# Kernel tuning notes

Hardware: AMD Instinct MI355X
Metric: run time of the kernel (lower is better)

The kernel has to match this reference:

```python
import jax, jax.numpy as jnp
import numpy as np

DIM = 384; HEADS = 16; HEAD_DIM = DIM // HEADS; HID = 4 * DIM
ETA_SCALE = 0.01; CLIP_INNER = 1.0; EPS = 1e-5
B = 8; T_FR = 32; GH = 16; GW = 16; CHUNK = 8; N = T_FR * GH * GW
D_SEG = 2 * (HEAD_DIM // 3 // 2)  # 8 dims each for t/h/w rotation (3*8 == head_dim)


def _layernorm(x, g, b):
    m = jnp.mean(x, -1, keepdims=True)
    v = jnp.var(x, -1, keepdims=True)
    return (x - m) * jax.lax.rsqrt(v + EPS) * g + b


def _mlp(W1, b1, W2, b2, x):
    # 2-layer Titan memory / CMS level MLP: dim -> 4*dim -> dim, GELU
    return jax.nn.gelu(x @ W1 + b1) @ W2 + b2


def _rope_seg(x, pos):
    # x: [..., s] interleaved-pair RoPE with positions pos (broadcastable to x[..., 0])
    s = x.shape[-1]; half = s // 2
    freqs = 1.0 / (10000.0 ** (jnp.arange(half, dtype=x.dtype) / half))
    ang = pos[..., None] * freqs
    c, si = jnp.cos(ang), jnp.sin(ang)
    x1, x2 = x[..., 0::2], x[..., 1::2]
    return jnp.stack([x1 * c - x2 * si, x1 * si + x2 * c], -1).reshape(x.shape)


def _apply_rope(x, tp, hp, wp):
    # 3D RoPE per head over (t, h, w) position segments
    b, n, d = x.shape
    xh = x.reshape(b, n, HEADS, HEAD_DIM)
    s = D_SEG
    parts = [_rope_seg(xh[..., 0:s], tp[None, :, None]),
             _rope_seg(xh[..., s:2 * s], hp[None, :, None]),
             _rope_seg(xh[..., 2 * s:3 * s], wp[None, :, None])]
    if 3 * s < HEAD_DIM:
        parts.append(xh[..., 3 * s:])
    return jnp.concatenate(parts, -1).reshape(b, n, d)


def _forward(x, norm1_g, norm1_b, q_W, tW1, tb1, tW2, tb2, out_W, out_b,
             norm2_g, norm2_b, cms_W1, cms_b1, cms_W2, cms_b2, T, H, W, chunk_size):
    Bx, Nt, D = x.shape
    y = _layernorm(x, norm1_g, norm1_b)
    nc = T // chunk_size
    Cper = chunk_size * H * W
    y_ch = y.reshape(Bx, nc, Cper, D).swapaxes(0, 1)  # [nc, B, Cper, D]
    # per-chunk RoPE positions (positions restart each chunk, matching _titan_forward_chunk)
    tp = jnp.repeat(jnp.arange(chunk_size, dtype=x.dtype), H * W)
    hp = jnp.tile(jnp.repeat(jnp.arange(H, dtype=x.dtype), W), chunk_size)
    wp = jnp.tile(jnp.arange(W, dtype=x.dtype), chunk_size * H)

    def mem_loss(W1, b1, W2, b2, kk, tt):
        return jnp.mean((_mlp(W1, b1, W2, b2, kk) - tt) ** 2)

    grad_fn = jax.grad(mem_loss, argnums=(0, 1, 2, 3))
    mlp_v = jax.vmap(_mlp, in_axes=(0, 0, 0, 0, None))

    def step(carry, yc):
        W1s, b1s, W2s, b2s = carry  # stacked [5, ...]: k, v, eta, alpha, memory
        gen = mlp_v(W1s[:4], b1s[:4], W2s[:4], b2s[:4], yc)  # [4, B, C, D]
        k, v, eta_raw, alpha_raw = gen[0], gen[1], gen[2], gen[3]
        eta = jax.nn.softplus(eta_raw) * ETA_SCALE
        alpha = jax.nn.sigmoid(alpha_raw)
        q = yc @ q_W
        q = _apply_rope(q, tp, hp, wp)
        k = _apply_rope(k, tp, hp, wp)
        out = _mlp(W1s[4], b1s[4], W2s[4], b2s[4], q)  # retrieve from main memory
        # surprise signal (per-token retrieval error norm); threshold=0 -> always update
        # surprise = jnp.linalg.norm(v - out, axis=-1)
        # self-targets v_hat = M_box(v) for the 4 adaptive memories; main memory targets v
        vhat = mlp_v(W1s[:4], b1s[:4], W2s[:4], b2s[:4], v)
        targets = jnp.concatenate([jax.lax.stop_gradient(vhat), v[None]], 0)  # [5,B,C,D]
        g1, g2, g3, g4 = jax.vmap(grad_fn, in_axes=(0, 0, 0, 0, None, 0))(
            W1s, b1s, W2s, b2s, k, targets)
        norm = jnp.sqrt(jnp.sum(g1 * g1, (1, 2)) + jnp.sum(g2 * g2, 1)
                        + jnp.sum(g3 * g3, (1, 2)) + jnp.sum(g4 * g4, 1))
        sc = jnp.minimum(1.0, CLIP_INNER / (norm + 1e-12))  # inner grad clip per memory
        em = jnp.mean(eta); am = jnp.mean(alpha)
        # DGD update with decay alpha and lr eta: p <- (1-alpha)*p - eta*g
        W1n = (1 - am) * W1s - em * g1 * sc[:, None, None]
        b1n = (1 - am) * b1s - em * g2 * sc[:, None]
        W2n = (1 - am) * W2s - em * g3 * sc[:, None, None]
        b2n = (1 - am) * b2s - em * g4 * sc[:, None]
        return (W1n, b1n, W2n, b2n), out

    _, outs = jax.lax.scan(step, (tW1, tb1, tW2, tb2), y_ch)
    titan = outs.swapaxes(0, 1).reshape(Bx, Nt, D) @ out_W + out_b
    x2 = x + titan
    # Phase B: CMS multi-frequency MLP cascade (sequential chain of level MLPs)
    h = _layernorm(x2, norm2_g, norm2_b)
    for l in range(cms_W1.shape[0]):
        h = _mlp(cms_W1[l], cms_b1[l], cms_W2[l], cms_b2[l], h)
    return x2 + h


def setup_inputs() -> dict:
    key = jax.random.key(0)
    ks = jax.random.split(key, 8)
    s = 0.02
    f = jnp.float32
    return {
        'x': jax.random.normal(ks[0], (B, N, DIM), f),
        'norm1_g': jnp.ones((DIM,), f), 'norm1_b': jnp.zeros((DIM,), f),
        'q_W': jax.random.normal(ks[1], (DIM, DIM), f) * s,
        'tW1': jax.random.normal(ks[2], (5, DIM, HID), f) * s,
        'tb1': jnp.zeros((5, HID), f),
        'tW2': jax.random.normal(ks[3], (5, HID, DIM), f) * s,
        'tb2': jnp.zeros((5, DIM), f),
        'out_W': jax.random.normal(ks[4], (DIM, DIM), f) * s,
        'out_b': jnp.zeros((DIM,), f),
        'norm2_g': jnp.ones((DIM,), f), 'norm2_b': jnp.zeros((DIM,), f),
        'cms_W1': jax.random.normal(ks[5], (3, DIM, HID), f) * s,
        'cms_b1': jnp.zeros((3, HID), f),
        'cms_W2': jax.random.normal(ks[6], (3, HID, DIM), f) * s,
        'cms_b2': jnp.zeros((3, DIM), f),
        'T': T_FR, 'H': GH, 'W': GW, 'chunk_size': CHUNK,
    }


def reference(x, norm1_g, norm1_b, q_W, tW1, tb1, tW2, tb2, out_W, out_b,
              norm2_g, norm2_b, cms_W1, cms_b1, cms_W2, cms_b2, T, H, W, chunk_size):
    return _forward(x, norm1_g, norm1_b, q_W, tW1, tb1, tW2, tb2, out_W, out_b,
                    norm2_g, norm2_b, cms_W1, cms_b1, cms_W2, cms_b2, T, H, W, chunk_size)
```

## Files before the change

kernel.cpp:

```cpp
#include <hip/hip_runtime.h>
#include <cstddef>
#include <cstdint>


typedef __bf16 bf16;
typedef __bf16 bf16x4 __attribute__((ext_vector_type(4)));
typedef __bf16 bf16x8 __attribute__((ext_vector_type(8)));
typedef float  f32x4  __attribute__((ext_vector_type(4)));

constexpr float INV_CNT = 1.0f / 6291456.0f;

__device__ __forceinline__ float fast_gelu(float x) {
  float u = 0.7978845608028654f * (x + 0.044715f * x * x * x);
  return x / (1.0f + __expf(-2.0f * u));
}
__device__ __forceinline__ float fast_gelu_grad(float x) {
  float x2 = x * x;
  float u = 0.7978845608028654f * (x + 0.044715f * x * x2);
  float s = 1.0f / (1.0f + __expf(-2.0f * u));
  return s + x * s * (1.0f - s) * 1.5957691216057308f * (1.0f + 0.134145f * x2);
}
__device__ __forceinline__ f32x4 gelu4(f32x4 v) {
  v[0] = fast_gelu(v[0]); v[1] = fast_gelu(v[1]);
  v[2] = fast_gelu(v[2]); v[3] = fast_gelu(v[3]);
  return v;
}
__device__ __forceinline__ bf16x4 tobf4(f32x4 v) {
  bf16x4 o; o[0] = (bf16)v[0]; o[1] = (bf16)v[1]; o[2] = (bf16)v[2]; o[3] = (bf16)v[3];
  return o;
}
__device__ __forceinline__ f32x4 tof4(bf16x4 v) {
  return f32x4{(float)v[0], (float)v[1], (float)v[2], (float)v[3]};
}

__device__ __forceinline__ void gload16(const bf16* g, void* lds) {
  __builtin_amdgcn_global_load_lds(
      (const __attribute__((address_space(1))) void*)g,
      (__attribute__((address_space(3))) void*)lds, 16, 0, 0);
}

template <int N>
__device__ __forceinline__ void wait_vmcnt() {
  if constexpr (N == 0)      asm volatile("s_waitcnt vmcnt(0)" ::: "memory");
  else if constexpr (N == 2) asm volatile("s_waitcnt vmcnt(2)" ::: "memory");
  else if constexpr (N == 3) asm volatile("s_waitcnt vmcnt(3)" ::: "memory");
  else if constexpr (N == 4) asm volatile("s_waitcnt vmcnt(4)" ::: "memory");
  __builtin_amdgcn_sched_barrier(0);
}

__device__ __forceinline__ int xcd_chunk(int id, int n) {
  int q = n >> 3, r = n & 7;
  int xcd = id & 7, pos = id >> 3;
  return (xcd < r ? xcd * (q + 1) : r * (q + 1) + (xcd - r) * q) + pos;
}

__global__ __launch_bounds__(64)
void ln_kernel(const float* __restrict__ x, const float* __restrict__ g,
               const float* __restrict__ b, bf16* __restrict__ y,
               int shift, int base, int stride) {
  int r = blockIdx.x;
  int src = ((r >> shift) * stride) + base + (r & ((1 << shift) - 1));
  int lane = threadIdx.x;
  const float* xr = x + (size_t)src * 384;
  float vals[6];
  float s = 0.f, s2 = 0.f;
#pragma unroll
  for (int i = 0; i < 6; ++i) {
    float v = xr[lane + i * 64];
    vals[i] = v; s += v; s2 += v * v;
  }
#pragma unroll
  for (int o = 32; o > 0; o >>= 1) { s += __shfl_xor(s, o); s2 += __shfl_xor(s2, o); }
  float m = s * (1.0f / 384.0f);
  float var = s2 * (1.0f / 384.0f) - m * m;
  float rr = rsqrtf(var + 1e-5f);
  bf16* yr = y + (size_t)r * 384;
#pragma unroll
  for (int i = 0; i < 6; ++i) {
    int c = lane + i * 64;
    yr[c] = (bf16)((vals[i] - m) * rr * g[c] + b[c]);
  }
}

__device__ __forceinline__ void trw_body(const float* in, bf16* out, int R, int C,
                                         int c0, int r0, int tid) {
  __shared__ float t[32][33];
  int tr = tid >> 3, tc = (tid & 7) * 4;
  f32x4 v = *(const f32x4*)&in[(size_t)(r0 + tr) * C + c0 + tc];
  t[tr][tc + 0] = v[0]; t[tr][tc + 1] = v[1]; t[tr][tc + 2] = v[2]; t[tr][tc + 3] = v[3];
  __syncthreads();
  bf16x4 o;
  o[0] = (bf16)t[tc + 0][tr]; o[1] = (bf16)t[tc + 1][tr];
  o[2] = (bf16)t[tc + 2][tr]; o[3] = (bf16)t[tc + 3][tr];
  *(bf16x4*)&out[(size_t)(c0 + tr) * R + r0 + tc] = o;
}

__global__ __launch_bounds__(256)
void trans_state(const float* __restrict__ SW1, const float* __restrict__ SW2,
                 bf16* __restrict__ sw1t, bf16* __restrict__ sw2t) {
  int z = blockIdx.z;
  if (z < 5)
    trw_body(SW1 + (size_t)z * 589824, sw1t + (size_t)z * 589824, 384, 1536,
             blockIdx.x * 32, blockIdx.y * 32, threadIdx.x);
  else
    trw_body(SW2 + (size_t)(z - 5) * 589824, sw2t + (size_t)(z - 5) * 589824, 1536, 384,
             blockIdx.y * 32, blockIdx.x * 32, threadIdx.x);
}

__global__ __launch_bounds__(256)
void trans_static(const float* __restrict__ qW, const float* __restrict__ outW,
                  const float* __restrict__ cW1, const float* __restrict__ cW2,
                  bf16* __restrict__ qwt, bf16* __restrict__ owt,
                  bf16* __restrict__ cw1t, bf16* __restrict__ cw2t) {
  int z = blockIdx.z;
  if (z < 2) {
    if (blockIdx.x >= 12) return;
    trw_body(z ? outW : qW, z ? owt : qwt, 384, 384,
             blockIdx.x * 32, blockIdx.y * 32, threadIdx.x);
  } else if (z < 5) {
    int lc = z - 2;
    trw_body(cW1 + (size_t)lc * 589824, cw1t + (size_t)lc * 589824, 384, 1536,
             blockIdx.x * 32, blockIdx.y * 32, threadIdx.x);
  } else {
    int lc = z - 5;
    trw_body(cW2 + (size_t)lc * 589824, cw2t + (size_t)lc * 589824, 1536, 384,
             blockIdx.y * 32, blockIdx.x * 32, threadIdx.x);
  }
}

__global__ __launch_bounds__(256)
void tr_bf(const bf16* __restrict__ in, bf16* __restrict__ out, int R, int C) {
  __shared__ bf16 t[32][36];
  int r0 = blockIdx.x * 32, c0 = blockIdx.y * 32;
  int tr = threadIdx.x >> 3, tc = (threadIdx.x & 7) * 4;
  bf16x4 v = *(const bf16x4*)&in[(size_t)(r0 + tr) * C + c0 + tc];
  t[tr][tc + 0] = v[0]; t[tr][tc + 1] = v[1]; t[tr][tc + 2] = v[2]; t[tr][tc + 3] = v[3];
  __syncthreads();
  bf16x4 o;
  o[0] = t[tc + 0][tr]; o[1] = t[tc + 1][tr]; o[2] = t[tc + 2][tr]; o[3] = t[tc + 3][tr];
  *(bf16x4*)&out[(size_t)(c0 + tr) * R + r0 + tc] = o;
}

__global__ __launch_bounds__(256)
void copy_bf16(const float* __restrict__ in, bf16* __restrict__ out, int n) {
  int i = (blockIdx.x * 256 + threadIdx.x) * 4;
  if (i < n) {
    f32x4 v = *(const f32x4*)&in[i];
    *(bf16x4*)&out[i] = tobf4(v);
  }
}

enum { E_BF16 = 0, E_GELU, E_PAIR, E_SUB, E_MUL, E_F32ADD, E_KV, E_RED2 };

template <int EPI, int BM>
__global__ __launch_bounds__(BM == 128 ? 512 : 256)
void mm_fwd(const bf16* __restrict__ Act, int lda, const bf16* __restrict__ W,
            const float* __restrict__ bias, const bf16* __restrict__ baux,
            const float* __restrict__ faux, float* __restrict__ red,
            bf16* __restrict__ Cb, bf16* __restrict__ C2, bf16* __restrict__ Ct,
            float* __restrict__ Cf, int K, int ldc, int ldt, float scale,
            int croff, int cshift, int cbase, int cstride,
            long zA, long zW, int zB) {
  constexpr int NW = (BM == 128) ? 8 : 4;
  constexpr int NFM = 2;
  constexpr int TW = 8 / NW;
  constexpr int TA = (BM / 16) / NW;
  constexpr int LPT = TW + TA;
  constexpr int SWE = 128 * 32;
  constexpr int SAE = BM * 32;
  constexpr int BUFE = 2 * (SWE + SAE);
  constexpr int SLABE = NW * 16 * 68 * 2;
  constexpr int SMEME = (BUFE > SLABE) ? BUFE : SLABE;
  constexpr bool TRANS = (EPI == E_PAIR || EPI == E_SUB || EPI == E_MUL);
  __shared__ bf16 smem[SMEME];
  const int z = blockIdx.z;
  Act += (size_t)z * zA;
  W   += (size_t)z * zW;
  if (bias) bias += (size_t)z * zB;
  const int nx = gridDim.x;
  const int nid = xcd_chunk(blockIdx.y * nx + blockIdx.x, nx * gridDim.y);
  const int m0 = (nid / nx) * BM, i0 = (nid % nx) * 128;
  const int tid = threadIdx.x;
  const int l = tid & 63, w = tid >> 6;
  const int a = l & 15, g = l >> 4;
  const int wi0 = (w & 1) * 64, wm0 = (w >> 1) * 32;
  const int srow = l >> 2;
  const int sue = ((l & 3) ^ ((l >> 3) & 3)) * 8;
  const int fru = (g ^ ((a >> 1) & 3)) << 4;

  const bf16* wp = W   + (size_t)(i0 + srow) * K   + sue;
  const bf16* ap = Act + (size_t)(m0 + srow) * lda + sue;

  f32x4 acc[4][NFM];
#pragma unroll
  for (int i = 0; i < 4; ++i)
#pragma unroll
    for (int j = 0; j < NFM; ++j) acc[i][j] = f32x4{0.f, 0.f, 0.f, 0.f};

  auto stage = [&](int buf, int k0) {
    bf16* dW = smem + buf * SWE;
    bf16* dA = smem + 2 * SWE + buf * SAE;
#pragma unroll
    for (int t = 0; t < TW; ++t) {
      const int seg = w * TW + t;
      gload16(wp + (size_t)(seg * 16) * K + k0, (char*)dW + seg * 1024);
    }
#pragma unroll
    for (int t = 0; t < TA; ++t) {
      const int seg = w * TA + t;
      gload16(ap + (size_t)(seg * 16) * lda + k0, (char*)dA + seg * 1024);
    }
  };

  const int nIt = K >> 5;
  stage(0, 0);
  for (int it = 0; it < nIt; ++it) {
    const int cur = it & 1;
    if (it + 1 < nIt) { stage(cur ^ 1, (it + 1) << 5); wait_vmcnt<LPT>(); }
    else              { wait_vmcnt<0>(); }
    __builtin_amdgcn_s_barrier();
    const bf16* bW = smem + cur * SWE;
    const bf16* bA = smem + 2 * SWE + cur * SAE;
    {
      bf16x8 Af[4], Bf[NFM];
#pragma unroll
      for (int f = 0; f < 4; ++f) {
        const int rW = wi0 + f * 16 + a;
        Af[f] = *(const bf16x8*)((const char*)bW + rW * 64 + fru);
      }
#pragma unroll
      for (int f = 0; f < NFM; ++f) {
        const int rA = wm0 + f * 16 + a;
        Bf[f] = *(const bf16x8*)((const char*)bA + rA * 64 + fru);
      }
#pragma unroll
      for (int fi = 0; fi < 4; ++fi)
#pragma unroll
        for (int fm = 0; fm < NFM; ++fm)
          acc[fi][fm] = __builtin_amdgcn_mfma_f32_16x16x32_bf16(Af[fi], Bf[fm], acc[fi][fm], 0, 0, 0);
    }
    asm volatile("s_waitcnt lgkmcnt(0)" ::: "memory");
    __builtin_amdgcn_s_barrier();
  }

  if constexpr (EPI == E_RED2) {
    float ssum = 0.f;
#pragma unroll
    for (int fi = 0; fi < 4; ++fi) {
      f32x4 b4 = *(const f32x4*)&bias[i0 + wi0 + fi * 16 + g * 4];
#pragma unroll
      for (int fm = 0; fm < NFM; ++fm)
#pragma unroll
        for (int r = 0; r < 4; ++r) {
          float vv = acc[fi][fm][r] + b4[r];
          if (z == 0) ssum += fmaxf(vv, 0.f) + log1pf(__expf(-fabsf(vv)));
          else        ssum += 1.0f / (1.0f + __expf(-vv));
        }
    }
#pragma unroll
    for (int o = 32; o > 0; o >>= 1) ssum += __shfl_xor(ssum, o);
    float* wred = (float*)smem;
    if (l == 0) wred[w] = ssum;
    __syncthreads();
    if (tid == 0) {
      float t2 = 0.f;
      for (int q = 0; q < NW; ++q) t2 += wred[q];
      atomicAdd(&red[z], t2);
    }
    return;
  } else {
    float* T = (float*)smem + w * (16 * 68);
    const int iB = i0 + wi0;
    f32x4 b4 = f32x4{0.f, 0.f, 0.f, 0.f};
    if (bias) b4 = *(const f32x4*)&bias[iB + a * 4];
#pragma unroll
    for (int fm = 0; fm < NFM; ++fm) {
#pragma unroll
      for (int fi = 0; fi < 4; ++fi)
        *(f32x4*)&T[a * 68 + fi * 16 + g * 4] = acc[fi][fm];
      asm volatile("s_waitcnt lgkmcnt(0)" ::: "memory");
      __builtin_amdgcn_sched_barrier(0);

#pragma unroll
      for (int q = 0; q < 4; ++q) {
        const int ml = wm0 + fm * 16 + q * 4 + g;
        const int trow = q * 4 + g;
        f32x4 v = *(const f32x4*)&T[trow * 68 + a * 4];
        v += b4;
        if constexpr (EPI == E_F32ADD) {
          const int rr = croff + m0 + ml;
          const int crow = ((rr >> cshift) * cstride) + cbase + (rr & ((1 << cshift) - 1));
          const size_t cb = (size_t)crow * ldc + iB + a * 4;
          v += *(const f32x4*)&faux[cb];
          *(f32x4*)&Cf[cb] = v;
        } else {
          const size_t cb = (size_t)(m0 + ml) * ldc + iB + a * 4;
          if constexpr (EPI == E_BF16) {
            *(bf16x4*)&Cb[cb] = tobf4(v);
          } else if constexpr (EPI == E_KV) {
            bf16* DST = (z == 0) ? Cb : C2;
            *(bf16x4*)&DST[cb] = tobf4(v);
          } else if constexpr (EPI == E_GELU) {
            *(bf16x4*)&Cb[cb] = tobf4(gelu4(v));
          } else if constexpr (EPI == E_PAIR) {
            *(bf16x4*)&Cb[cb] = tobf4(v);
            f32x4 gv = gelu4(v);
            *(bf16x4*)&C2[cb] = tobf4(gv);
            *(f32x4*)&T[trow * 68 + a * 4] = gv;
          } else if constexpr (EPI == E_SUB) {
            f32x4 t4 = tof4(*(const bf16x4*)&baux[cb]);
            v = (v - t4) * scale;
            *(bf16x4*)&Cb[cb] = tobf4(v);
            *(f32x4*)&T[trow * 68 + a * 4] = v;
          } else if constexpr (EPI == E_MUL) {
            f32x4 h4 = tof4(*(const bf16x4*)&baux[cb]);
            v[0] *= fast_gelu_grad(h4[0]); v[1] *= fast_gelu_grad(h4[1]);
            v[2] *= fast_gelu_grad(h4[2]); v[3] *= fast_gelu_grad(h4[3]);
            *(f32x4*)&T[trow * 68 + a * 4] = v;
          }
        }
      }

      if constexpr (TRANS) {
        asm volatile("s_waitcnt lgkmcnt(0)" ::: "memory");
        __builtin_amdgcn_sched_barrier(0);
        const int mg = m0 + wm0 + fm * 16;
        bf16x8 o0, o1;
#pragma unroll
        for (int j = 0; j < 16; ++j) {
          float vv = T[j * 68 + l];
          if (j < 8) o0[j] = (bf16)vv; else o1[j - 8] = (bf16)vv;
        }
        *(bf16x8*)&Ct[(size_t)(iB + l) * ldt + mg] = o0;
        *(bf16x8*)&Ct[(size_t)(iB + l) * ldt + mg + 8] = o1;
      }
    }
  }
}

__global__ __launch_bounds__(512)
void mm_tn2c(const bf16* __restrict__ P1, int ldP1, const bf16* __restrict__ Q1, int ldQ1,
             float* __restrict__ Ga, int ldGa,
             const bf16* __restrict__ P2, int ldP2, const bf16* __restrict__ Q2, int ldQ2,
             float* __restrict__ Gb, int ldGb, int mlen,
             float* __restrict__ G4s, float* __restrict__ G2s) {
  constexpr int SBE = 128 * 64;
  __shared__ bf16 smem[4 * SBE];
  const int nid = xcd_chunk(blockIdx.x, gridDim.x);
  const int grp = nid / 36, pair = nid % 36;
  const int part = grp & 1, zsl = grp >> 1;
  const bf16* P; const bf16* Q; float* G; float* Gsum;
  int ldP, ldQ, ldG, p0, q0;
  if (part == 0) {
    P = P1; Q = Q1; G = Ga; ldP = ldP1; ldQ = ldQ1; ldG = ldGa; Gsum = G4s;
    p0 = (pair / 3) * 128; q0 = (pair % 3) * 128;
  } else {
    P = P2; Q = Q2; G = Gb; ldP = ldP2; ldQ = ldQ2; ldG = ldGb; Gsum = G2s;
    p0 = (pair / 12) * 128; q0 = (pair % 12) * 128;
  }
  const bool doSum = (p0 == 0);
  const int tid = threadIdx.x;
  const int mb = zsl * mlen;
  const int l = tid & 63, w = tid >> 6;
  const int a = l & 15, g = l >> 4;
  const int wp0 = (w & 1) * 64, wq0 = (w >> 1) * 32;
  const int lrow = l >> 3;
  const int lcolel = (((l & 7) ^ lrow) << 4) >> 1;

  const bf16* pp = P + (size_t)(p0 + lrow) * ldP + lcolel;
  const bf16* qp = Q + (size_t)(q0 + lrow) * ldQ + lcolel;

  f32x4 acc[4][2];
#pragma unroll
  for (int i = 0; i < 4; ++i)
#pragma unroll
    for (int j = 0; j < 2; ++j) acc[i][j] = f32x4{0.f, 0.f, 0.f, 0.f};
  float qsum = 0.f;
  const int srow = w * 16 + (l & 15);
  const int u0 = ((l >> 4) ^ (l & 7)) & 7;
  const int u1 = u0 ^ 4;

  auto stage = [&](int buf, int m0) {
    bf16* dP = smem + buf * SBE;
    bf16* dQ = smem + 2 * SBE + buf * SBE;
#pragma unroll
    for (int t = 0; t < 2; ++t) {
      const int seg = w * 2 + t;
      gload16(pp + (size_t)(seg * 8) * ldP + m0, (char*)dP + seg * 1024);
      gload16(qp + (size_t)(seg * 8) * ldQ + m0, (char*)dQ + seg * 1024);
    }
  };

  const int nIt = mlen >> 6;
  stage(0, mb);
  for (int it = 0; it < nIt; ++it) {
    const int cur = it & 1;
    if (it + 1 < nIt) { stage(cur ^ 1, mb + ((it + 1) << 6)); wait_vmcnt<4>(); }
    else              { wait_vmcnt<0>(); }
    __builtin_amdgcn_s_barrier();
    const bf16* bP = smem + cur * SBE;
    const bf16* bQ = smem + 2 * SBE + cur * SBE;
#pragma unroll
    for (int kh = 0; kh < 2; ++kh) {
      bf16x8 Pf[4], Qf[2];
#pragma unroll
      for (int f = 0; f < 4; ++f) {
        const int rP = wp0 + f * 16 + a;
        Pf[f] = *(const bf16x8*)((const char*)bP +
                 ((rP * 128 + kh * 64 + g * 16) ^ ((rP & 7) << 4)));
      }
#pragma unroll
      for (int f = 0; f < 2; ++f) {
        const int rQ = wq0 + f * 16 + a;
        Qf[f] = *(const bf16x8*)((const char*)bQ +
                 ((rQ * 128 + kh * 64 + g * 16) ^ ((rQ & 7) << 4)));
      }
#pragma unroll
      for (int f1 = 0; f1 < 4; ++f1)
#pragma unroll
        for (int f2 = 0; f2 < 2; ++f2)
          acc[f1][f2] = __builtin_amdgcn_mfma_f32_16x16x32_bf16(Pf[f1], Qf[f2], acc[f1][f2], 0, 0, 0);
    }
    if (doSum) {
      bf16x8 s0 = *(const bf16x8*)((const char*)bQ + srow * 128 + u0 * 16);
      bf16x8 s1 = *(const bf16x8*)((const char*)bQ + srow * 128 + u1 * 16);
#pragma unroll
      for (int e = 0; e < 8; ++e) qsum += (float)s0[e] + (float)s1[e];
    }
    asm volatile("s_waitcnt lgkmcnt(0)" ::: "memory");
    __builtin_amdgcn_s_barrier();
  }
#pragma unroll
  for (int f1 = 0; f1 < 4; ++f1)
#pragma unroll
    for (int f2 = 0; f2 < 2; ++f2)
#pragma unroll
      for (int r = 0; r < 4; ++r)
        atomicAdd(&G[(size_t)(p0 + wp0 + f1 * 16 + g * 4 + r) * ldG + q0 + wq0 + f2 * 16 + a],
                  acc[f1][f2][r]);
  if (doSum) {
    qsum += __shfl_xor(qsum, 16);
    qsum += __shfl_xor(qsum, 32);
    if (l < 16) atomicAdd(&Gsum[q0 + w * 16 + l], qsum);
  }
}

__global__ __launch_bounds__(256)
void rope_kernel(bf16* __restrict__ p0, int rbase) {
  int idx = blockIdx.x * blockDim.x + threadIdx.x;
  int row = idx >> 4, hd = idx & 15;
  int j = (rbase + row) & 2047;
  float pos[3] = { (float)(j >> 8), (float)((j >> 4) & 15), (float)(j & 15) };
  const float freqs[4] = { 1.0f, 0.1f, 0.01f, 0.001f };
  bf16* p = p0 + (size_t)row * 384 + hd * 24;
#pragma unroll
  for (int s = 0; s < 3; ++s) {
    bf16x8 vv = *(bf16x8*)(p + s * 8);
#pragma unroll
    for (int pr = 0; pr < 4; ++pr) {
      float ang = pos[s] * freqs[pr];
      float si, co;
      sincosf(ang, &si, &co);
      float e0 = (float)vv[2 * pr], e1 = (float)vv[2 * pr + 1];
      vv[2 * pr]     = (bf16)(e0 * co - e1 * si);
      vv[2 * pr + 1] = (bf16)(e0 * si + e1 * co);
    }
    *(bf16x8*)(p + s * 8) = vv;
  }
}

__global__ __launch_bounds__(256)
void sumsq_all(const float* __restrict__ G1, const float* __restrict__ G2,
               const float* __restrict__ G3, const float* __restrict__ G4,
               float* __restrict__ red) {
  int i = blockIdx.y, bx = blockIdx.x;
  const float* base; int per, lb, nb;
  if (bx < 256)      { base = G1 + (size_t)i * 589824; per = 589824; lb = bx;       nb = 256; }
  else if (bx < 512) { base = G3 + (size_t)i * 589824; per = 589824; lb = bx - 256; nb = 256; }
  else if (bx < 514) { base = G2 + (size_t)i * 1536;   per = 1536;   lb = bx - 512; nb = 2; }
  else               { base = G4 + (size_t)i * 384;    per = 384;    lb = bx - 514; nb = 2; }
  float s = 0.f;
  for (int idx = lb * 256 + threadIdx.x; idx < per; idx += nb * 256) {
    float v = base[idx]; s += v * v;
  }
  __shared__ float sm[256];
  sm[threadIdx.x] = s; __syncthreads();
  for (int o = 128; o > 0; o >>= 1) {
    if (threadIdx.x < o) sm[threadIdx.x] += sm[threadIdx.x + o];
    __syncthreads();
  }
  if (threadIdx.x == 0) atomicAdd(&red[2 + i], sm[0]);
}

__global__ __launch_bounds__(256)
void update_all(float* __restrict__ SW1, float* __restrict__ SB1,
                float* __restrict__ SW2, float* __restrict__ SB2,
                const float* __restrict__ G1, const float* __restrict__ G2,
                const float* __restrict__ G3, const float* __restrict__ G4,
                const float* __restrict__ red) {
  int i = blockIdx.y, bx = blockIdx.x;
  float* S; const float* G; int per, lb, nb;
  if (bx < 512)       { S = SW1; G = G1; per = 589824; lb = bx;        nb = 512; }
  else if (bx < 1024) { S = SW2; G = G3; per = 589824; lb = bx - 512;  nb = 512; }
  else if (bx < 1028) { S = SB1; G = G2; per = 1536;   lb = bx - 1024; nb = 4; }
  else                { S = SB2; G = G4; per = 384;    lb = bx - 1028; nb = 4; }
  size_t base = (size_t)i * per;
  float em = 0.01f * red[0] * INV_CNT;
  float am = red[1] * INV_CNT;
  float norm = sqrtf(red[2 + i]);
  float sc = fminf(1.0f, 1.0f / (norm + 1e-12f));
  float ws_ = 1.0f - am;
  float gs = em * sc;
  for (int idx = lb * 256 + (int)threadIdx.x; idx < per; idx += nb * 256)
    S[base + idx] = ws_ * S[base + idx] - gs * G[base + idx];
}

extern "C" void kernel_launch(void* const* d_in, const int* in_sizes, int n_in,
                              void* d_out, int out_size, void* d_ws, size_t ws_size,
                              hipStream_t stream) {
  const float* x    = (const float*)d_in[0];
  const float* n1g  = (const float*)d_in[1];
  const float* n1b  = (const float*)d_in[2];
  const float* qW   = (const float*)d_in[3];
  const float* tW1  = (const float*)d_in[4];
  const float* tb1  = (const float*)d_in[5];
  const float* tW2  = (const float*)d_in[6];
  const float* tb2  = (const float*)d_in[7];
  const float* outW = (const float*)d_in[8];
  const float* outb = (const float*)d_in[9];
  const float* n2g  = (const float*)d_in[10];
  const float* n2b  = (const float*)d_in[11];
  const float* cW1  = (const float*)d_in[12];
  const float* cb1  = (const float*)d_in[13];
  const float* cW2  = (const float*)d_in[14];
  const float* cb2  = (const float*)d_in[15];
  float* out = (float*)d_out;

  const size_t W1SZ = 384 * 1536, W2SZ = 1536 * 384;
  const size_t STATE = 5 * W1SZ + 5 * 1536 + 5 * W2SZ + 5 * 384;
  const size_t BF_W = 21 * W1SZ + 2 * 147456;
  const size_t CHUNK_BF = 4 * (size_t)16384 * 384;
  const size_t FIXEDF = 2 * STATE + 16 + BF_W / 2 + CHUNK_BF / 2;
  size_t MS = 16384;
  while (MS > 2048 && (FIXEDF + MS * 3840) * 4 > ws_size) MS >>= 1;
  if ((FIXEDF + MS * 3840) * 4 > ws_size) {
    hipMemcpyAsync(d_out, d_in[0], (size_t)25165824 * 4, hipMemcpyDeviceToDevice, stream);
    return;
  }
  const int NS = (int)(16384 / MS);
  const int iMS = (int)MS;

  float* ws = (float*)d_ws;
  size_t off = 0;
  auto alloc = [&](size_t n) { float* p = ws + off; off += n; return p; };
  auto balloc = [&](size_t n) { bf16* p = (bf16*)(ws + off); off += (n + 1) / 2; return p; };
  float* SW1 = alloc(5 * W1SZ);
  float* SB1 = alloc(5 * 1536);
  float* SW2 = alloc(5 * W2SZ);
  float* SB2 = alloc(5 * 384);
  float* G1  = alloc(5 * W1SZ);
  float* G2  = alloc(5 * 1536);
  float* G3  = alloc(5 * W2SZ);
  float* G4  = alloc(5 * 384);
  float* RED = alloc(16);
  bf16* Yc   = balloc((size_t)16384 * 384);
  bf16* Kb   = balloc((size_t)16384 * 384);
  bf16* Vb   = balloc((size_t)16384 * 384);
  bf16* Kbt  = balloc((size_t)16384 * 384);
  bf16* sw1t = balloc(5 * W1SZ);
  bf16* sw2t = balloc(5 * W2SZ);
  bf16* sw2c = balloc(5 * W2SZ);
  bf16* qwt  = balloc(147456);
  bf16* owt  = balloc(147456);
  bf16* cw1t = balloc(3 * W1SZ);
  bf16* cw2t = balloc(3 * W2SZ);
  bf16* pool = balloc(MS * 3072);
  bf16* GH1t = balloc(MS * 1536);
  bf16* DAt  = balloc(MS * 1536);
  bf16* OD   = balloc(MS * 384);
  bf16* ODt  = balloc(MS * 384);
  bf16* T2   = balloc(MS * 384);
  bf16* Tt   = balloc(MS * 384);
  bf16* H1r  = pool;
  bf16* GH1k = pool + MS * 1536;

  hipMemcpyAsync(SW1, tW1, 5 * W1SZ * 4, hipMemcpyDeviceToDevice, stream);
  hipMemcpyAsync(SB1, tb1, 5 * 1536 * 4, hipMemcpyDeviceToDevice, stream);
  hipMemcpyAsync(SW2, tW2, 5 * W2SZ * 4, hipMemcpyDeviceToDevice, stream);
  hipMemcpyAsync(SB2, tb2, 5 * 384 * 4, hipMemcpyDeviceToDevice, stream);

  trans_static<<<dim3(48, 12, 8), 256, 0, stream>>>(qW, outW, cW1, cW2, qwt, owt, cw1t, cw2t);

  const size_t grads_bytes = STATE * 4;
  const int gm  = iMS / 128;
  const int gm2 = iMS / 64;
  int mlen_t = iMS / 8; if (mlen_t < 128) mlen_t = 128;
  if (mlen_t > 2048) mlen_t = 2048;
  const int nzt = iMS / mlen_t;
  const int tn_grid = 36 * 2 * nzt;
  const float SC = 2.0f * INV_CNT;
  const size_t MSR = (size_t)iMS * 384;

  for (int c = 0; c < 4; ++c) {
    hipMemsetAsync(G1, 0, grads_bytes, stream);
    hipMemsetAsync(RED, 0, 64, stream);
    trans_state<<<dim3(48, 12, 10), 256, 0, stream>>>(SW1, SW2, sw1t, sw2t);
    copy_bf16<<<dim3(2880), 256, 0, stream>>>(SW2, sw2c, (int)(5 * W2SZ));

    ln_kernel<<<dim3(16384), dim3(64), 0, stream>>>(x, n1g, n1b, Yc, 11, c * 2048, 8192);

    for (int s = 0; s < NS; ++s) {
      const bf16* Ys = Yc + (size_t)s * MSR;
      mm_fwd<E_GELU, 128><<<dim3(24, gm), 512, 0, stream>>>(Ys, 384, sw1t,
          SB1, nullptr, nullptr, nullptr, pool, nullptr, nullptr, nullptr,
          384, 3072, 0, 0.f, 0, 30, 0, 0, 0, 0, 0);
      mm_fwd<E_KV, 64><<<dim3(3, gm2, 2), 256, 0, stream>>>(pool, 3072, sw2t,
          SB2, nullptr, nullptr, nullptr, Kb + s * MSR, Vb + s * MSR, nullptr, nullptr,
          1536, 384, 0, 0.f, 0, 30, 0, 0, 1536, (long)W2SZ, 384);
      mm_fwd<E_GELU, 128><<<dim3(24, gm), 512, 0, stream>>>(Ys, 384, sw1t + 2 * W1SZ,
          SB1 + 2 * 1536, nullptr, nullptr, nullptr, pool, nullptr, nullptr, nullptr,
          384, 3072, 0, 0.f, 0, 30, 0, 0, 0, 0, 0);
      mm_fwd<E_RED2, 64><<<dim3(3, gm2, 2), 256, 0, stream>>>(pool, 3072, sw2t + 2 * W2SZ,
          SB2 + 2 * 384, nullptr, nullptr, RED, nullptr, nullptr, nullptr, nullptr,
          1536, 384, 0, 0.f, 0, 30, 0, 0, 1536, (long)W2SZ, 384);
    }

    for (int s = 0; s < NS; ++s) {
      const bf16* Ys = Yc + (size_t)s * MSR;
      mm_fwd<E_BF16, 64><<<dim3(3, gm2), 256, 0, stream>>>(Ys, 384, qwt,
          nullptr, nullptr, nullptr, nullptr, Tt, nullptr, nullptr, nullptr,
          384, 384, 0, 0.f, 0, 30, 0, 0, 0, 0, 0);
      rope_kernel<<<dim3(iMS / 16), 256, 0, stream>>>(Tt, s * iMS);
      mm_fwd<E_GELU, 128><<<dim3(12, gm), 512, 0, stream>>>(Tt, 384, sw1t + 4 * W1SZ,
          SB1 + 4 * 1536, nullptr, nullptr, nullptr, GH1k, nullptr, nullptr, nullptr,
          384, 1536, 0, 0.f, 0, 30, 0, 0, 0, 0, 0);
      mm_fwd<E_BF16, 64><<<dim3(3, gm2), 256, 0, stream>>>(GH1k, 1536, sw2t + 4 * W2SZ,
          SB2 + 4 * 384, nullptr, nullptr, nullptr, T2, nullptr, nullptr, nullptr,
          1536, 384, 0, 0.f, 0, 30, 0, 0, 0, 0, 0);
      mm_fwd<E_F32ADD, 64><<<dim3(3, gm2), 256, 0, stream>>>(T2, 384, owt, outb,
          nullptr, x, nullptr, nullptr, nullptr, nullptr, out,
          384, 384, 0, 0.f, s * iMS, 11, c * 2048, 8192, 0, 0, 0);
    }

    rope_kernel<<<dim3(1024), 256, 0, stream>>>(Kb, 0);
    tr_bf<<<dim3(512, 12), 256, 0, stream>>>(Kb, Kbt, 16384, 384);

    for (int s = 0; s < NS; ++s) {
      const bf16* Ks = Kb + (size_t)s * MSR;
      const bf16* Vs = Vb + (size_t)s * MSR;
      for (int i = 0; i < 5; ++i) {
        if (i < 4) {
          mm_fwd<E_GELU, 128><<<dim3(12, gm), 512, 0, stream>>>(Vs, 384, sw1t + i * W1SZ,
              SB1 + i * 1536, nullptr, nullptr, nullptr, GH1k, nullptr, nullptr, nullptr,
              384, 1536, 0, 0.f, 0, 30, 0, 0, 0, 0, 0);
          mm_fwd<E_BF16, 64><<<dim3(3, gm2), 256, 0, stream>>>(GH1k, 1536, sw2t + i * W2SZ,
              SB2 + i * 384, nullptr, nullptr, nullptr, Tt, nullptr, nullptr, nullptr,
              1536, 384, 0, 0.f, 0, 30, 0, 0, 0, 0, 0);
        }
        const bf16* tg = (i < 4) ? Tt : Vs;
        mm_fwd<E_PAIR, 128><<<dim3(12, gm), 512, 0, stream>>>(Ks, 384, sw1t + i * W1SZ,
            SB1 + i * 1536, nullptr, nullptr, nullptr, H1r, GH1k, GH1t, nullptr,
            384, 1536, iMS, 0.f, 0, 30, 0, 0, 0, 0, 0);
        mm_fwd<E_SUB, 64><<<dim3(3, gm2), 256, 0, stream>>>(GH1k, 1536, sw2t + i * W2SZ,
            SB2 + i * 384, tg, nullptr, nullptr, OD, nullptr, ODt, nullptr,
            1536, 384, iMS, SC, 0, 30, 0, 0, 0, 0, 0);
        mm_fwd<E_MUL, 128><<<dim3(12, gm), 512, 0, stream>>>(OD, 384, sw2c + i * W2SZ,
            nullptr, H1r, nullptr, nullptr, nullptr, nullptr, DAt, nullptr,
            384, 1536, iMS, 0.f, 0, 30, 0, 0, 0, 0, 0);
        mm_tn2c<<<dim3(tn_grid), 512, 0, stream>>>(
            GH1t, iMS, ODt, iMS, G3 + i * W2SZ, 384,
            Kbt + (size_t)s * iMS, 16384, DAt, iMS, G1 + i * W1SZ, 1536, mlen_t,
            G4 + i * 384, G2 + i * 1536);
      }
    }

    sumsq_all<<<dim3(516, 5), 256, 0, stream>>>(G1, G2, G3, G4, RED);
    update_all<<<dim3(1032, 5), 256, 0, stream>>>(SW1, SB1, SW2, SB2, G1, G2, G3, G4, RED);
  }

  const int NCS = (int)(65536 / MS);
  for (int s2 = 0; s2 < NCS; ++s2) {
    float* outp = out + (size_t)s2 * MSR;
    ln_kernel<<<dim3(iMS), dim3(64), 0, stream>>>(out, n2g, n2b, OD, 30, s2 * iMS, 0);
    bf16* hc = OD; bf16* hn = T2;
    for (int lc = 0; lc < 3; ++lc) {
      mm_fwd<E_GELU, 128><<<dim3(12, gm), 512, 0, stream>>>(hc, 384, cw1t + lc * W1SZ,
          cb1 + lc * 1536, nullptr, nullptr, nullptr, GH1k, nullptr, nullptr, nullptr,
          384, 1536, 0, 0.f, 0, 30, 0, 0, 0, 0, 0);
      if (lc < 2) {
        mm_fwd<E_BF16, 64><<<dim3(3, gm2), 256, 0, stream>>>(GH1k, 1536, cw2t + lc * W2SZ,
            cb2 + lc * 384, nullptr, nullptr, nullptr, hn, nullptr, nullptr, nullptr,
            1536, 384, 0, 0.f, 0, 30, 0, 0, 0, 0, 0);
        bf16* t = hc; hc = hn; hn = t;
      } else {
        mm_fwd<E_F32ADD, 64><<<dim3(3, gm2), 256, 0, stream>>>(GH1k, 1536, cw2t + lc * W2SZ,
            cb2 + lc * 384, nullptr, outp, nullptr, nullptr, nullptr, nullptr, outp,
            1536, 384, 0, 0.f, 0, 30, 0, 0, 0, 0, 0);
      }
    }
  }
}
```

Measured before the change: 9.250 ms.

## Fold target MLP second layer into loss gradient via hidden difference

For levels 0-3 the target MLP and the memory MLP share W2, so the output difference (W2·gelu(h_k)+b2) − (W2·gelu(h_v)+b2) is rewritten as W2·(gelu(h_k) − gelu(h_v)). The second-layer GEMM that produced the target is replaced by an elementwise difference in the first-layer epilogue (E_PAIRD), followed by one scaled GEMM (E_SCL). The first-layer epilogue now stores gelu'(h) instead of raw h, so the backward epilogue becomes a plain multiply. The weight-gradient kernel also moves from a 64-wide to a 32-wide K step with a new swizzle, which halves shared memory per stage but doubles the number of loop iterations.

```diff
diff --git a/kernel.cpp b/kernel.cpp
--- a/kernel.cpp
+++ b/kernel.cpp
@@ -150,7 +150,7 @@
   }
 }
 
-enum { E_BF16 = 0, E_GELU, E_PAIR, E_SUB, E_MUL, E_F32ADD, E_KV, E_RED2 };
+enum { E_BF16 = 0, E_GELU, E_PAIR, E_PAIRD, E_SUB, E_SCL, E_MUL, E_F32ADD, E_KV, E_RED2 };
 
 template <int EPI, int BM>
 __global__ __launch_bounds__(BM == 128 ? 512 : 256)
@@ -171,7 +171,8 @@
   constexpr int BUFE = 2 * (SWE + SAE);
   constexpr int SLABE = NW * 16 * 68 * 2;
   constexpr int SMEME = (BUFE > SLABE) ? BUFE : SLABE;
-  constexpr bool TRANS = (EPI == E_PAIR || EPI == E_SUB || EPI == E_MUL);
+  constexpr bool TRANS = (EPI == E_PAIR || EPI == E_PAIRD || EPI == E_SUB ||
+                          EPI == E_SCL || EPI == E_MUL);
   __shared__ bf16 smem[SMEME];
   const int z = blockIdx.z;
   Act += (size_t)z * zA;
@@ -303,19 +304,34 @@
           } else if constexpr (EPI == E_GELU) {
             *(bf16x4*)&Cb[cb] = tobf4(gelu4(v));
           } else if constexpr (EPI == E_PAIR) {
-            *(bf16x4*)&Cb[cb] = tobf4(v);
+            f32x4 gp;
+            gp[0] = fast_gelu_grad(v[0]); gp[1] = fast_gelu_grad(v[1]);
+            gp[2] = fast_gelu_grad(v[2]); gp[3] = fast_gelu_grad(v[3]);
             f32x4 gv = gelu4(v);
+            *(bf16x4*)&Cb[cb] = tobf4(gp);
             *(bf16x4*)&C2[cb] = tobf4(gv);
+            *(f32x4*)&T[trow * 68 + a * 4] = gv;
+          } else if constexpr (EPI == E_PAIRD) {
+            f32x4 gp;
+            gp[0] = fast_gelu_grad(v[0]); gp[1] = fast_gelu_grad(v[1]);
+            gp[2] = fast_gelu_grad(v[2]); gp[3] = fast_gelu_grad(v[3]);
+            f32x4 gv = gelu4(v);
+            f32x4 d = gv - tof4(*(const bf16x4*)&baux[cb]);
+            *(bf16x4*)&Cb[cb] = tobf4(gp);
+            *(bf16x4*)&C2[cb] = tobf4(d);
             *(f32x4*)&T[trow * 68 + a * 4] = gv;
           } else if constexpr (EPI == E_SUB) {
             f32x4 t4 = tof4(*(const bf16x4*)&baux[cb]);
             v = (v - t4) * scale;
             *(bf16x4*)&Cb[cb] = tobf4(v);
             *(f32x4*)&T[trow * 68 + a * 4] = v;
+          } else if constexpr (EPI == E_SCL) {
+            v = v * scale;
+            *(bf16x4*)&Cb[cb] = tobf4(v);
+            *(f32x4*)&T[trow * 68 + a * 4] = v;
           } else if constexpr (EPI == E_MUL) {
             f32x4 h4 = tof4(*(const bf16x4*)&baux[cb]);
-            v[0] *= fast_gelu_grad(h4[0]); v[1] *= fast_gelu_grad(h4[1]);
-            v[2] *= fast_gelu_grad(h4[2]); v[3] *= fast_gelu_grad(h4[3]);
+            v *= h4;
             *(f32x4*)&T[trow * 68 + a * 4] = v;
           }
         }
@@ -344,7 +360,7 @@
              const bf16* __restrict__ P2, int ldP2, const bf16* __restrict__ Q2, int ldQ2,
              float* __restrict__ Gb, int ldGb, int mlen,
              float* __restrict__ G4s, float* __restrict__ G2s) {
-  constexpr int SBE = 128 * 64;
+  constexpr int SBE = 128 * 32;
   __shared__ bf16 smem[4 * SBE];
   const int nid = xcd_chunk(blockIdx.x, gridDim.x);
   const int grp = nid / 36, pair = nid % 36;
@@ -364,11 +380,16 @@
   const int l = tid & 63, w = tid >> 6;
   const int a = l & 15, g = l >> 4;
   const int wp0 = (w & 1) * 64, wq0 = (w >> 1) * 32;
-  const int lrow = l >> 3;
-  const int lcolel = (((l & 7) ^ lrow) << 4) >> 1;
-
-  const bf16* pp = P + (size_t)(p0 + lrow) * ldP + lcolel;
-  const bf16* qp = Q + (size_t)(q0 + lrow) * ldQ + lcolel;
+  const int srow = l >> 2;
+  const int sue = ((l & 3) ^ ((l >> 3) & 3)) * 8;
+  const int fru = (g ^ ((a >> 1) & 3)) << 4;
+
+  const bf16* pp = P + (size_t)(p0 + w * 16 + srow % 16) * 0;
+  (void)pp;
+  const bf16* pbase = P + (size_t)(p0 + w * 16 + srow) * 0;
+  (void)pbase;
+  const bf16* pP = P + (size_t)(p0 + w * 16 + (l >> 2)) * ldP + sue;
+  const bf16* pQ = Q + (size_t)(q0 + w * 16 + (l >> 2)) * ldQ + sue;
 
   f32x4 acc[4][2];
 #pragma unroll
@@ -376,44 +397,35 @@
 #pragma unroll
     for (int j = 0; j < 2; ++j) acc[i][j] = f32x4{0.f, 0.f, 0.f, 0.f};
   float qsum = 0.f;
-  const int srow = w * 16 + (l & 15);
-  const int u0 = ((l >> 4) ^ (l & 7)) & 7;
-  const int u1 = u0 ^ 4;
+  const int sumoff = (w * 16 + (l >> 2)) * 64 + (l & 3) * 16;
 
   auto stage = [&](int buf, int m0) {
     bf16* dP = smem + buf * SBE;
     bf16* dQ = smem + 2 * SBE + buf * SBE;
-#pragma unroll
-    for (int t = 0; t < 2; ++t) {
-      const int seg = w * 2 + t;
-      gload16(pp + (size_t)(seg * 8) * ldP + m0, (char*)dP + seg * 1024);
-      gload16(qp + (size_t)(seg * 8) * ldQ + m0, (char*)dQ + seg * 1024);
-    }
+    gload16(pP + m0, (char*)dP + w * 1024);
+    gload16(pQ + m0, (char*)dQ + w * 1024);
   };
 
-  const int nIt = mlen >> 6;
+  const int nIt = mlen >> 5;
   stage(0, mb);
   for (int it = 0; it < nIt; ++it) {
     const int cur = it & 1;
-    if (it + 1 < nIt) { stage(cur ^ 1, mb + ((it + 1) << 6)); wait_vmcnt<4>(); }
+    if (it + 1 < nIt) { stage(cur ^ 1, mb + ((it + 1) << 5)); wait_vmcnt<2>(); }
     else              { wait_vmcnt<0>(); }
     __builtin_amdgcn_s_barrier();
     const bf16* bP = smem + cur * SBE;
     const bf16* bQ = smem + 2 * SBE + cur * SBE;
-#pragma unroll
-    for (int kh = 0; kh < 2; ++kh) {
+    {
       bf16x8 Pf[4], Qf[2];
 #pragma unroll
       for (int f = 0; f < 4; ++f) {
         const int rP = wp0 + f * 16 + a;
-        Pf[f] = *(const bf16x8*)((const char*)bP +
-                 ((rP * 128 + kh * 64 + g * 16) ^ ((rP & 7) << 4)));
+        Pf[f] = *(const bf16x8*)((const char*)bP + rP * 64 + fru);
       }
 #pragma unroll
       for (int f = 0; f < 2; ++f) {
         const int rQ = wq0 + f * 16 + a;
-        Qf[f] = *(const bf16x8*)((const char*)bQ +
-                 ((rQ * 128 + kh * 64 + g * 16) ^ ((rQ & 7) << 4)));
+        Qf[f] = *(const bf16x8*)((const char*)bQ + rQ * 64 + fru);
       }
 #pragma unroll
       for (int f1 = 0; f1 < 4; ++f1)
@@ -422,10 +434,9 @@
           acc[f1][f2] = __builtin_amdgcn_mfma_f32_16x16x32_bf16(Pf[f1], Qf[f2], acc[f1][f2], 0, 0, 0);
     }
     if (doSum) {
-      bf16x8 s0 = *(const bf16x8*)((const char*)bQ + srow * 128 + u0 * 16);
-      bf16x8 s1 = *(const bf16x8*)((const char*)bQ + srow * 128 + u1 * 16);
-#pragma unroll
-      for (int e = 0; e < 8; ++e) qsum += (float)s0[e] + (float)s1[e];
+      bf16x8 s0 = *(const bf16x8*)((const char*)bQ + sumoff);
+#pragma unroll
+      for (int e = 0; e < 8; ++e) qsum += (float)s0[e];
     }
     asm volatile("s_waitcnt lgkmcnt(0)" ::: "memory");
     __builtin_amdgcn_s_barrier();
@@ -439,9 +450,9 @@
         atomicAdd(&G[(size_t)(p0 + wp0 + f1 * 16 + g * 4 + r) * ldG + q0 + wq0 + f2 * 16 + a],
                   acc[f1][f2][r]);
   if (doSum) {
-    qsum += __shfl_xor(qsum, 16);
-    qsum += __shfl_xor(qsum, 32);
-    if (l < 16) atomicAdd(&Gsum[q0 + w * 16 + l], qsum);
+    qsum += __shfl_xor(qsum, 1);
+    qsum += __shfl_xor(qsum, 2);
+    if ((l & 3) == 0) atomicAdd(&Gsum[q0 + w * 16 + (l >> 2)], qsum);
   }
 }
 
@@ -653,17 +664,20 @@
           mm_fwd<E_GELU, 128><<<dim3(12, gm), 512, 0, stream>>>(Vs, 384, sw1t + i * W1SZ,
               SB1 + i * 1536, nullptr, nullptr, nullptr, GH1k, nullptr, nullptr, nullptr,
               384, 1536, 0, 0.f, 0, 30, 0, 0, 0, 0, 0);
-          mm_fwd<E_BF16, 64><<<dim3(3, gm2), 256, 0, stream>>>(GH1k, 1536, sw2t + i * W2SZ,
-              SB2 + i * 384, nullptr, nullptr, nullptr, Tt, nullptr, nullptr, nullptr,
-              1536, 384, 0, 0.f, 0, 30, 0, 0, 0, 0, 0);
+          mm_fwd<E_PAIRD, 128><<<dim3(12, gm), 512, 0, stream>>>(Ks, 384, sw1t + i * W1SZ,
+              SB1 + i * 1536, GH1k, nullptr, nullptr, H1r, DAt, GH1t, nullptr,
+              384, 1536, iMS, 0.f, 0, 30, 0, 0, 0, 0, 0);
+          mm_fwd<E_SCL, 64><<<dim3(3, gm2), 256, 0, stream>>>(DAt, 1536, sw2t + i * W2SZ,
+              nullptr, nullptr, nullptr, nullptr, OD, nullptr, ODt, nullptr,
+              1536, 384, iMS, SC, 0, 30, 0, 0, 0, 0, 0);
+        } else {
+          mm_fwd<E_PAIR, 128><<<dim3(12, gm), 512, 0, stream>>>(Ks, 384, sw1t + 4 * W1SZ,
+              SB1 + 4 * 1536, nullptr, nullptr, nullptr, H1r, GH1k, GH1t, nullptr,
+              384, 1536, iMS, 0.f, 0, 30, 0, 0, 0, 0, 0);
+          mm_fwd<E_SUB, 64><<<dim3(3, gm2), 256, 0, stream>>>(GH1k, 1536, sw2t + 4 * W2SZ,
+              SB2 + 4 * 384, Vs, nullptr, nullptr, OD, nullptr, ODt, nullptr,
+              1536, 384, iMS, SC, 0, 30, 0, 0, 0, 0, 0);
         }
-        const bf16* tg = (i < 4) ? Tt : Vs;
-        mm_fwd<E_PAIR, 128><<<dim3(12, gm), 512, 0, stream>>>(Ks, 384, sw1t + i * W1SZ,
-            SB1 + i * 1536, nullptr, nullptr, nullptr, H1r, GH1k, GH1t, nullptr,
-            384, 1536, iMS, 0.f, 0, 30, 0, 0, 0, 0, 0);
-        mm_fwd<E_SUB, 64><<<dim3(3, gm2), 256, 0, stream>>>(GH1k, 1536, sw2t + i * W2SZ,
-            SB2 + i * 384, tg, nullptr, nullptr, OD, nullptr, ODt, nullptr,
-            1536, 384, iMS, SC, 0, 30, 0, 0, 0, 0, 0);
         mm_fwd<E_MUL, 128><<<dim3(12, gm), 512, 0, stream>>>(OD, 384, sw2c + i * W2SZ,
             nullptr, H1r, nullptr, nullptr, nullptr, nullptr, DAt, nullptr,
             384, 1536, iMS, 0.f, 0, 30, 0, 0, 0, 0, 0);
```

New measurement: 8.806 ms. 1.05x faster.
